# Kernel optimization log

Measured on AMD Instinct MI355X. Metric: run time of the kernel, lower is better.

## Reference

```python
import jax, jax.numpy as jnp
import numpy as np

ROPE_BASE = 10000.0
NUM_HEADS = 16
NUM_KV_HEADS = 4


def _rms_norm(x, eps):
    # F.rms_norm with no weight: x / sqrt(mean(x^2) + eps)
    return x * jax.lax.rsqrt(jnp.mean(x * x, axis=-1, keepdims=True) + eps)


def _apply_rope(x, cos, sin):
    h = x.shape[-1] // 2
    x1, x2 = x[..., :h], x[..., h:]
    return jnp.concatenate([x1 * cos + x2 * sin, -x1 * sin + x2 * cos], axis=-1)


def setup_inputs() -> dict:
    key = jax.random.key(0)
    ks = jax.random.split(key, 5)
    B, T, D = 2, 2048, 1024
    H, Hkv = NUM_HEADS, NUM_KV_HEADS
    hd = D // H
    kv_dim = Hkv * hd
    s_in = 1.0 / np.sqrt(D)
    return {
        "x": jax.random.normal(ks[0], (B, T, D), dtype=jnp.float32),
        "Wq": jax.random.normal(ks[1], (D, D), dtype=jnp.float32) * s_in,
        "Wk": jax.random.normal(ks[2], (kv_dim, D), dtype=jnp.float32) * s_in,
        "Wv": jax.random.normal(ks[3], (kv_dim, D), dtype=jnp.float32) * s_in,
        "Wproj": jax.random.normal(ks[4], (D, D), dtype=jnp.float32) * s_in,
        "q_gain": jnp.full((H,), 1.0, dtype=jnp.float32),
    }


def reference(x, Wq, Wk, Wv, Wproj, q_gain):
    B, T, D = x.shape
    H, Hkv = NUM_HEADS, NUM_KV_HEADS
    hd = D // H
    rep = H // Hkv
    eps = jnp.finfo(x.dtype).eps

    # QKV projections (F.linear: x @ W.T)
    q = jnp.einsum('btd,od->bto', x, Wq).reshape(B, T, H, hd).transpose(0, 2, 1, 3)
    k = jnp.einsum('btd,od->bto', x, Wk).reshape(B, T, Hkv, hd).transpose(0, 2, 1, 3)
    v = jnp.einsum('btd,od->bto', x, Wv).reshape(B, T, Hkv, hd).transpose(0, 2, 1, 3)

    q = _rms_norm(q, eps)
    k = _rms_norm(k, eps)

    # RoPE tables: [1, 1, T, hd/2]
    inv_freq = 1.0 / (ROPE_BASE ** (jnp.arange(0, hd, 2, dtype=jnp.float32) / hd))
    f = jnp.arange(T, dtype=jnp.float32)[:, None] * inv_freq[None, :]
    cos = jnp.cos(f)[None, None].astype(q.dtype)
    sin = jnp.sin(f)[None, None].astype(q.dtype)
    q = _apply_rope(q, cos, sin)
    k = _apply_rope(k, cos, sin)

    q = q * q_gain.astype(q.dtype)[None, :, None, None]

    # GQA without materializing repeated K/V: group q heads [Hkv, rep]
    qg = q.reshape(B, Hkv, rep, T, hd)
    scale = hd ** -0.5
    scores = jnp.einsum('bgrqd,bgkd->bgrqk', qg, k) * scale
    causal = jnp.tril(jnp.ones((T, T), dtype=bool))
    scores = jnp.where(causal, scores, -jnp.inf)
    att = jax.nn.softmax(scores.astype(jnp.float32), axis=-1).astype(q.dtype)
    y = jnp.einsum('bgrqk,bgkd->bgrqd', att, v)  # [B,Hkv,rep,T,hd]
    y = y.reshape(B, H, T, hd).transpose(0, 2, 1, 3).reshape(B, T, D)
    return jnp.einsum('btd,od->bto', y, Wproj)
```

## Files before the change

kernel.cpp:

```cpp
#include <hip/hip_runtime.h>
#include <cstdint>
#include <cstddef>

typedef __attribute__((ext_vector_type(8))) short short8;
typedef __attribute__((ext_vector_type(4))) float floatx4;
typedef __attribute__((ext_vector_type(4))) short short4v;
typedef unsigned short u16;
typedef unsigned int u32;

#define B_   2
#define T_   2048
#define D_   1024
#define H_   16
#define HKV_ 4
#define HD_  64
#define KV_  256
#define M_   4096
#define QS_  1536

#define NX   4194304
#define NWQ  1048576
#define NWK  262144
#define NWV  262144
#define NWP  1048576
#define NCAST (NX + NWQ + NWK + NWV + NWP)
#define CAST_BLOCKS (NCAST / 1024)
#define TAB_BLOCKS  256

__device__ __forceinline__ float b2f(u16 u) {
    union { u32 i; float f; } v; v.i = ((u32)u) << 16; return v.f;
}
__device__ __forceinline__ u16 f2b(float f) {
    union { float f; u32 i; } v; v.f = f;
    u32 r = v.i + 0x7FFF + ((v.i >> 16) & 1);
    return (u16)(r >> 16);
}
__device__ __forceinline__ u32 pack_hi(float a, float b) {
    union { float f; u32 u; } ua, ub; ua.f = a; ub.f = b;
    return (ua.u >> 16) | (ub.u & 0xFFFF0000u);
}

__device__ __forceinline__ void async16(const u16* g, u16* l) {
    __builtin_amdgcn_global_load_lds(
        (const __attribute__((address_space(1))) u32*)g,
        (__attribute__((address_space(3))) u32*)l, 16, 0, 0);
}

__global__ __launch_bounds__(256) void prep(const float* __restrict__ x,
                                            const float* __restrict__ wq,
                                            const float* __restrict__ wk,
                                            const float* __restrict__ wv,
                                            const float* __restrict__ wp,
                                            u16* __restrict__ dst,
                                            float2* __restrict__ tab) {
    int blk = blockIdx.x;
    if (blk < CAST_BLOCKS) {
        int i = blk * 1024 + threadIdx.x * 4;
        const float* src; int off;
        if      (i < NX)                  { src = x;  off = i; }
        else if (i < NX+NWQ)              { src = wq; off = i - NX; }
        else if (i < NX+NWQ+NWK)          { src = wk; off = i - (NX+NWQ); }
        else if (i < NX+NWQ+NWK+NWV)      { src = wv; off = i - (NX+NWQ+NWK); }
        else                              { src = wp; off = i - (NX+NWQ+NWK+NWV); }
        float4 v = *(const float4*)(src + off);
        short4v o;
        o.x = (short)f2b(v.x); o.y = (short)f2b(v.y);
        o.z = (short)f2b(v.z); o.w = (short)f2b(v.w);
        *(short4v*)(dst + i) = o;
    } else {
        int idx = (blk - CAST_BLOCKS) * 256 + threadIdx.x;
        int t = idx >> 5, i = idx & 31;
        float freq = exp2f(-(float)i * (13.287712379549449f / 32.0f));
        float ang = (float)t * freq;
        tab[idx] = make_float2(cosf(ang), sinf(ang));
    }
}

__global__ __launch_bounds__(256, 3) void gemm_qkv(const u16* __restrict__ A,
                                                   const u16* __restrict__ W,
                                                   u16* __restrict__ C,
                                                   u16* __restrict__ Vt,
                                                   const float* __restrict__ gain,
                                                   const float2* __restrict__ tab) {
    const int K = D_;
    __shared__ u16 As[2][2][128 * 32];
    __shared__ u16 Bs[2][2][64 * 32];
    const int t = threadIdx.x;
    const int wave = t >> 6, lane = t & 63;
    const int quad = lane >> 4, l16 = lane & 15;
    const int wm = wave * 32;
    const int m0 = blockIdx.y * 128, n0 = blockIdx.x * 64;

    floatx4 acc[2][4];
#pragma unroll
    for (int i = 0; i < 2; i++)
#pragma unroll
        for (int j = 0; j < 4; j++) acc[i][j] = (floatx4){0.f, 0.f, 0.f, 0.f};

    const int sr = t >> 2, sc = (t & 3) * 8;
    const u16* ga = A + (size_t)(m0 + sr) * K + sc;
    const u16* gb = W + (size_t)(n0 + sr) * K + sc;

    auto stage = [&](int buf, int half, int koff) {
        async16(ga + koff, As[buf][half] + t * 8);
        async16(ga + koff + (size_t)64 * K, As[buf][half] + t * 8 + 64 * 32);
        async16(gb + koff, Bs[buf][half] + t * 8);
    };

    stage(0, 0, 0);
    stage(0, 1, 32);

    int cur = 0;
    for (int kt = 0; kt < K; kt += 64) {
        __syncthreads();
        if (kt + 64 < K) {
            stage(cur ^ 1, 0, kt + 64);
            stage(cur ^ 1, 1, kt + 96);
        }
#pragma unroll
        for (int half = 0; half < 2; half++) {
            short8 af[2], bf[4];
#pragma unroll
            for (int mt = 0; mt < 2; mt++)
                af[mt] = *(const short8*)(As[cur][half] + (wm + mt * 16 + l16) * 32 + quad * 8);
#pragma unroll
            for (int nt = 0; nt < 4; nt++)
                bf[nt] = *(const short8*)(Bs[cur][half] + (nt * 16 + l16) * 32 + quad * 8);
#pragma unroll
            for (int mt = 0; mt < 2; mt++)
#pragma unroll
                for (int nt = 0; nt < 4; nt++)
                    acc[mt][nt] = __builtin_amdgcn_mfma_f32_16x16x32_bf16(
                        af[mt], bf[nt], acc[mt][nt], 0, 0, 0);
        }
        cur ^= 1;
    }

    const int col0 = n0;
    if (col0 < 1280) {
        float gs = (col0 < 1024)
                 ? gain[col0 >> 6] * (0.125f * 1.4426950408889634f)
                 : 1.0f;
#pragma unroll
        for (int mt = 0; mt < 2; mt++)
#pragma unroll
            for (int r = 0; r < 4; r++) {
                int row = m0 + wm + mt * 16 + quad * 4 + r;
                int tt = row & (T_ - 1);
                float v0 = acc[mt][0][r], v1 = acc[mt][1][r];
                float v2 = acc[mt][2][r], v3 = acc[mt][3][r];
                float ss = v0 * v0 + v1 * v1 + v2 * v2 + v3 * v3;
                ss += __shfl_xor(ss, 1); ss += __shfl_xor(ss, 2);
                ss += __shfl_xor(ss, 4); ss += __shfl_xor(ss, 8);
                float inv = rsqrtf(ss * (1.0f / 64.0f) + 1.1920929e-7f);
                v0 *= inv; v1 *= inv; v2 *= inv; v3 *= inv;
                float2 cs0 = tab[tt * 32 + l16];
                float2 cs1 = tab[tt * 32 + 16 + l16];
                float o0 = (v0 * cs0.x + v2 * cs0.y) * gs;
                float o1 = (v1 * cs1.x + v3 * cs1.y) * gs;
                float o2 = (v2 * cs0.x - v0 * cs0.y) * gs;
                float o3 = (v3 * cs1.x - v1 * cs1.y) * gs;
                u16* cp = C + (size_t)row * QS_ + col0 + l16;
                cp[0]  = f2b(o0);
                cp[16] = f2b(o1);
                cp[32] = f2b(o2);
                cp[48] = f2b(o3);
            }
    } else {
        const int g = (col0 - 1280) >> 6;
#pragma unroll
        for (int mt = 0; mt < 2; mt++)
#pragma unroll
            for (int r = 0; r < 4; r++) {
                int row = m0 + wm + mt * 16 + quad * 4 + r;
                int tt = row & (T_ - 1);
                int bb = row >> 11;
#pragma unroll
                for (int nt = 0; nt < 4; nt++)
                    Vt[(size_t)((bb * 4 + g) * 64 + nt * 16 + l16) * T_ + tt] =
                        f2b(acc[mt][nt][r]);
            }
    }
}

__global__ __launch_bounds__(256, 3) void gemm_proj(const u16* __restrict__ A,
                                                    const u16* __restrict__ W,
                                                    float* __restrict__ C) {
    const int K = D_;
    __shared__ u16 As[2][2][128 * 32];
    __shared__ u16 Bs[2][2][64 * 32];
    const int t = threadIdx.x;
    const int wave = t >> 6, lane = t & 63;
    const int quad = lane >> 4, l16 = lane & 15;
    const int wm = wave * 32;
    const int m0 = blockIdx.y * 128, n0 = blockIdx.x * 64;

    floatx4 acc[2][4];
#pragma unroll
    for (int i = 0; i < 2; i++)
#pragma unroll
        for (int j = 0; j < 4; j++) acc[i][j] = (floatx4){0.f, 0.f, 0.f, 0.f};

    const int sr = t >> 2, sc = (t & 3) * 8;
    const u16* ga = A + (size_t)(m0 + sr) * K + sc;
    const u16* gb = W + (size_t)(n0 + sr) * K + sc;

    auto stage = [&](int buf, int half, int koff) {
        async16(ga + koff, As[buf][half] + t * 8);
        async16(ga + koff + (size_t)64 * K, As[buf][half] + t * 8 + 64 * 32);
        async16(gb + koff, Bs[buf][half] + t * 8);
    };

    stage(0, 0, 0);
    stage(0, 1, 32);

    int cur = 0;
    for (int kt = 0; kt < K; kt += 64) {
        __syncthreads();
        if (kt + 64 < K) {
            stage(cur ^ 1, 0, kt + 64);
            stage(cur ^ 1, 1, kt + 96);
        }
#pragma unroll
        for (int half = 0; half < 2; half++) {
            short8 af[2], bf[4];
#pragma unroll
            for (int mt = 0; mt < 2; mt++)
                af[mt] = *(const short8*)(As[cur][half] + (wm + mt * 16 + l16) * 32 + quad * 8);
#pragma unroll
            for (int nt = 0; nt < 4; nt++)
                bf[nt] = *(const short8*)(Bs[cur][half] + (nt * 16 + l16) * 32 + quad * 8);
#pragma unroll
            for (int mt = 0; mt < 2; mt++)
#pragma unroll
                for (int nt = 0; nt < 4; nt++)
                    acc[mt][nt] = __builtin_amdgcn_mfma_f32_16x16x32_bf16(
                        af[mt], bf[nt], acc[mt][nt], 0, 0, 0);
        }
        cur ^= 1;
    }

#pragma unroll
    for (int mt = 0; mt < 2; mt++)
#pragma unroll
        for (int nt = 0; nt < 4; nt++)
#pragma unroll
            for (int r = 0; r < 4; r++) {
                int row = m0 + wm + mt * 16 + quad * 4 + r;
                int col = n0 + nt * 16 + l16;
                C[(size_t)row * D_ + col] = acc[mt][nt][r];
            }
}

__global__ __launch_bounds__(256, 4) void flash(const u16* __restrict__ QKV,
                                                const u16* __restrict__ Vtr,
                                                u16* __restrict__ Y,
                                                float* __restrict__ Opart,
                                                float* __restrict__ Lpart) {
    const int u  = blockIdx.x;
    const int h  = blockIdx.y;
    const int b  = blockIdx.z;
    const int g  = h >> 2;
    const int w    = threadIdx.x >> 6;
    const int lane = threadIdx.x & 63;
    const int quad = lane >> 4, l16 = lane & 15;

    __shared__ u16 Kt[64 * 64];
    __shared__ u16 Vs[64 * 64];
    __shared__ __align__(16) u16 P[4][16][72];

    const int xp = u & 15;
    const int nseg = (u < 16) ? 2 : 1;
    const int buf  = (u < 16) ? 0 : 1;
    int m0s[2], k0s[2], k1s[2];
    if (u < 16) {
        m0s[0] = xp * 64;        k0s[0] = 0;  k1s[0] = xp + 1;
        m0s[1] = (31 - xp) * 64; k0s[1] = 16; k1s[1] = 32 - xp;
    } else {
        m0s[0] = (31 - xp) * 64; k0s[0] = 0;  k1s[0] = 16;
        m0s[1] = 0; k0s[1] = 0; k1s[1] = 0;
    }

    const int srow = w * 16 + (lane >> 3);
    const int sseg = (lane & 7) ^ ((lane >> 3) & 7);
    const u16* kgb = QKV + (size_t)(b * T_ + srow) * QS_ + D_ + g * 64 + sseg * 8;
    const u16* vgb = Vtr + (size_t)((b * 4 + g) * 64 + srow) * T_ + sseg * 8;
    u16* klds = Kt + w * 1024 + lane * 8;
    u16* vlds = Vs + w * 1024 + lane * 8;
    const int sw0 = (quad ^ (l16 & 7)) * 8;
    const int sw1 = ((4 + quad) ^ (l16 & 7)) * 8;

    auto stage = [&](int tile) {
        const u16* kg = kgb + (size_t)tile * 64 * QS_;
        const u16* vg = vgb + (size_t)tile * 64;
        async16(kg, klds);
        async16(kg + (size_t)8 * QS_, klds + 512);
        async16(vg, vlds);
        async16(vg + (size_t)8 * T_, vlds + 512);
    };

    short8 ones;
#pragma unroll
    for (int i = 0; i < 8; i++) ones[i] = (short)0x3F80;

    stage(k0s[0]);

    for (int seg = 0; seg < nseg; ++seg) {
        const int mseg = m0s[seg], k0 = k0s[seg], k1 = k1s[seg];
        const int jt = mseg >> 6;
        const int m = mseg + w * 16;

        const u16* qp = QKV + (size_t)(b * T_ + m + l16) * QS_ + h * HD_ + quad * 8;
        short8 aq0 = *(const short8*)(qp);
        short8 aq1 = *(const short8*)(qp + 32);

        floatx4 acc[4];
#pragma unroll
        for (int i = 0; i < 4; i++) acc[i] = (floatx4){0.f, 0.f, 0.f, 0.f};
        floatx4 lAcc = (floatx4){0.f, 0.f, 0.f, 0.f};

        for (int tk = k0; tk < k1; ++tk) {
            __syncthreads();

            floatx4 S[4];
#pragma unroll
            for (int nt = 0; nt < 4; nt++) {
                const u16* kr = Kt + (nt * 16 + l16) * 64;
                short8 kf0 = *(const short8*)(kr + sw0);
                short8 kf1 = *(const short8*)(kr + sw1);
                S[nt] = (floatx4){0.f, 0.f, 0.f, 0.f};
                S[nt] = __builtin_amdgcn_mfma_f32_16x16x32_bf16(kf0, aq0, S[nt], 0, 0, 0);
                S[nt] = __builtin_amdgcn_mfma_f32_16x16x32_bf16(kf1, aq1, S[nt], 0, 0, 0);
            }
            short8 vf[4][2];
#pragma unroll
            for (int dd = 0; dd < 4; dd++) {
                const u16* vr = Vs + (dd * 16 + l16) * 64;
                vf[dd][0] = *(const short8*)(vr + sw0);
                vf[dd][1] = *(const short8*)(vr + sw1);
            }
            __syncthreads();

            int nxt = (tk + 1 < k1) ? tk + 1 : ((seg + 1 < nseg) ? k0s[seg + 1] : -1);
            if (nxt >= 0) stage(nxt);

            const bool msk = (tk == jt);
            const int qq = m + l16;
#pragma unroll
            for (int nt = 0; nt < 4; nt++) {
                float p[4];
#pragma unroll
                for (int r = 0; r < 4; r++) {
                    float e = __builtin_amdgcn_exp2f(S[nt][r]);
                    if (msk) {
                        int key = tk * 64 + nt * 16 + quad * 4 + r;
                        e = (key <= qq) ? e : 0.f;
                    }
                    p[r] = e;
                }
                uint2 pw; pw.x = pack_hi(p[0], p[1]); pw.y = pack_hi(p[2], p[3]);
                *(uint2*)&P[w][l16][nt * 16 + quad * 4] = pw;
            }
            short8 pf0 = *(const short8*)&P[w][l16][quad * 8];
            short8 pf1 = *(const short8*)&P[w][l16][quad * 8 + 32];
#pragma unroll
            for (int dd = 0; dd < 4; dd++) {
                acc[dd] = __builtin_amdgcn_mfma_f32_16x16x32_bf16(pf0, vf[dd][0], acc[dd], 0, 0, 0);
                acc[dd] = __builtin_amdgcn_mfma_f32_16x16x32_bf16(pf1, vf[dd][1], acc[dd], 0, 0, 0);
            }
            lAcc = __builtin_amdgcn_mfma_f32_16x16x32_bf16(pf0, ones, lAcc, 0, 0, 0);
            lAcc = __builtin_amdgcn_mfma_f32_16x16x32_bf16(pf1, ones, lAcc, 0, 0, 0);
        }

        if (u < 16 && seg == 0) {
#pragma unroll
            for (int r = 0; r < 4; r++) {
                float inv = 1.0f / lAcc[r];
                int row = m + quad * 4 + r;
                u16* yp = Y + (size_t)(b * T_ + row) * D_ + h * HD_ + l16;
#pragma unroll
                for (int dd = 0; dd < 4; dd++)
                    yp[dd * 16] = f2b(acc[dd][r] * inv);
            }
        } else {
#pragma unroll
            for (int r = 0; r < 4; r++) {
                int rp = m + quad * 4 + r - 1024;
                float* op = Opart + ((size_t)((buf * 2 + b) * 1024 + rp)) * 1024
                          + h * HD_ + l16;
#pragma unroll
                for (int dd = 0; dd < 4; dd++)
                    op[dd * 16] = acc[dd][r];
                if (l16 == 0)
                    Lpart[((buf * 2 + b) * 1024 + rp) * 16 + h] = lAcc[r];
            }
        }
    }
}

__global__ __launch_bounds__(256) void combine(const float* __restrict__ Opart,
                                               const float* __restrict__ Lpart,
                                               u16* __restrict__ Y) {
    int e = (blockIdx.x * 256 + threadIdx.x) * 4;
    int b = e >> 20;
    int rem = e & 1048575;
    int row = rem >> 10, col = rem & 1023;
    int li = (b * 1024 + row) * 16 + (col >> 6);
    float l0 = Lpart[li];
    float l1 = Lpart[li + 2 * 1024 * 16];
    float inv = 1.0f / (l0 + l1);
    size_t oi = ((size_t)(b * 1024 + row)) * 1024 + col;
    float4 o0 = *(const float4*)(Opart + oi);
    float4 o1 = *(const float4*)(Opart + oi + (size_t)2 * 1024 * 1024);
    short4v y;
    y.x = (short)f2b((o0.x + o1.x) * inv); y.y = (short)f2b((o0.y + o1.y) * inv);
    y.z = (short)f2b((o0.z + o1.z) * inv); y.w = (short)f2b((o0.w + o1.w) * inv);
    *(short4v*)(Y + (size_t)(b * T_ + 1024 + row) * D_ + col) = y;
}

extern "C" void kernel_launch(void* const* d_in, const int* in_sizes, int n_in,
                              void* d_out, int out_size, void* d_ws, size_t ws_size,
                              hipStream_t stream) {
    const float* x    = (const float*)d_in[0];
    const float* Wq   = (const float*)d_in[1];
    const float* Wk   = (const float*)d_in[2];
    const float* Wv   = (const float*)d_in[3];
    const float* Wp   = (const float*)d_in[4];
    const float* gain = (const float*)d_in[5];
    float* out = (float*)d_out;

    u16* xb   = (u16*)d_ws;
    u16* Wcat = xb + (size_t)NX;
    u16* Wpb  = Wcat + (size_t)(NWQ + NWK + NWV);
    u16* QKV  = Wpb + (size_t)NWP;
    u16* Vt   = QKV + (size_t)M_ * QS_;
    u16* Y    = Vt + (size_t)M_ * KV_;
    float2* tab = (float2*)(Y + (size_t)M_ * D_);
    float* Opart = (float*)(tab + 65536);
    float* Lpart = Opart + (size_t)4 * 1024 * 1024;

    prep<<<CAST_BLOCKS + TAB_BLOCKS, 256, 0, stream>>>(x, Wq, Wk, Wv, Wp, xb, tab);

    gemm_qkv<<<dim3(QS_ / 64, M_ / 128), 256, 0, stream>>>(xb, Wcat, QKV, Vt,
                                                           gain, tab);

    flash<<<dim3(32, H_, B_), 256, 0, stream>>>(QKV, Vt, Y, Opart, Lpart);

    combine<<<2048, 256, 0, stream>>>(Opart, Lpart, Y);

    gemm_proj<<<dim3(D_ / 64, M_ / 128), 256, 0, stream>>>(Y, Wpb, out);
}
```

Measured before the change: 158.9 us.

## Rework flash attention with 32x32 MFMA, 128-row blocks and triple-buffered K/V

The flash kernel now processes 128 query rows per block, each wave handling 32 rows with 32x32x16 bf16 MFMA. P is repacked in registers via cvt_pk and permlane32 swaps instead of going through LDS, and the row sum is accumulated in scalar adds rather than an extra MFMA. K/V tiles are triple-buffered with explicit vmcnt waits and MFMA regions are raised with setprio. Each block pairs a short and a long causal segment. Both segments are always written as partials through an LDS-transposed coalesced store, so combine now runs over all rows. This trades more partial-output traffic and lower occupancy (launch bounds 2) for fewer LDS round trips and larger MFMA tiles.

```diff
diff --git a/kernel.cpp b/kernel.cpp
--- a/kernel.cpp
+++ b/kernel.cpp
@@ -4,6 +4,7 @@
 
 typedef __attribute__((ext_vector_type(8))) short short8;
 typedef __attribute__((ext_vector_type(4))) float floatx4;
+typedef __attribute__((ext_vector_type(16))) float floatx16;
 typedef __attribute__((ext_vector_type(4))) short short4v;
 typedef unsigned short u16;
 typedef unsigned int u32;
@@ -44,6 +45,23 @@
     __builtin_amdgcn_global_load_lds(
         (const __attribute__((address_space(1))) u32*)g,
         (__attribute__((address_space(3))) u32*)l, 16, 0, 0);
+}
+
+__device__ __forceinline__ u32 cvtpk(float lo, float hi) {
+    u32 r;
+    asm("v_cvt_pk_bf16_f32 %0, %1, %2" : "=v"(r) : "v"(lo), "v"(hi));
+    return r;
+}
+__device__ __forceinline__ void swap32(u32& a, u32& b) {
+    asm volatile("v_permlane32_swap_b32 %0, %1" : "+v"(a), "+v"(b));
+}
+__device__ __forceinline__ void swap32f(float& a, float& b) {
+    asm volatile("v_permlane32_swap_b32 %0, %1" : "+v"(a), "+v"(b));
+}
+__device__ __forceinline__ short8 pkfrag(u32 w0, u32 w1, u32 w2, u32 w3) {
+    union { u32 w[4]; short8 s; } u;
+    u.w[0] = w0; u.w[1] = w1; u.w[2] = w2; u.w[3] = w3;
+    return u.s;
 }
 
 __global__ __launch_bounds__(256) void prep(const float* __restrict__ x,
@@ -252,9 +270,8 @@
             }
 }
 
-__global__ __launch_bounds__(256, 4) void flash(const u16* __restrict__ QKV,
+__global__ __launch_bounds__(256, 2) void flash(const u16* __restrict__ QKV,
                                                 const u16* __restrict__ Vtr,
-                                                u16* __restrict__ Y,
                                                 float* __restrict__ Opart,
                                                 float* __restrict__ Lpart) {
     const int u  = blockIdx.x;
@@ -263,138 +280,165 @@
     const int g  = h >> 2;
     const int w    = threadIdx.x >> 6;
     const int lane = threadIdx.x & 63;
-    const int quad = lane >> 4, l16 = lane & 15;
-
-    __shared__ u16 Kt[64 * 64];
-    __shared__ u16 Vs[64 * 64];
-    __shared__ __align__(16) u16 P[4][16][72];
-
-    const int xp = u & 15;
-    const int nseg = (u < 16) ? 2 : 1;
-    const int buf  = (u < 16) ? 0 : 1;
-    int m0s[2], k0s[2], k1s[2];
-    if (u < 16) {
-        m0s[0] = xp * 64;        k0s[0] = 0;  k1s[0] = xp + 1;
-        m0s[1] = (31 - xp) * 64; k0s[1] = 16; k1s[1] = 32 - xp;
-    } else {
-        m0s[0] = (31 - xp) * 64; k0s[0] = 0;  k1s[0] = 16;
-        m0s[1] = 0; k0s[1] = 0; k1s[1] = 0;
-    }
+    const int ln31 = lane & 31;
+    const int hi   = lane >> 5;
+    const int swz  = lane & 7;
+
+    __shared__ u16 Kb[3][4096];
+    __shared__ u16 Vb[3][4096];
+    __shared__ float Ot[4][2048];
 
     const int srow = w * 16 + (lane >> 3);
     const int sseg = (lane & 7) ^ ((lane >> 3) & 7);
     const u16* kgb = QKV + (size_t)(b * T_ + srow) * QS_ + D_ + g * 64 + sseg * 8;
     const u16* vgb = Vtr + (size_t)((b * 4 + g) * 64 + srow) * T_ + sseg * 8;
-    u16* klds = Kt + w * 1024 + lane * 8;
-    u16* vlds = Vs + w * 1024 + lane * 8;
-    const int sw0 = (quad ^ (l16 & 7)) * 8;
-    const int sw1 = ((4 + quad) ^ (l16 & 7)) * 8;
-
-    auto stage = [&](int tile) {
+
+    auto stage = [&](int tile, int bi) {
         const u16* kg = kgb + (size_t)tile * 64 * QS_;
         const u16* vg = vgb + (size_t)tile * 64;
-        async16(kg, klds);
-        async16(kg + (size_t)8 * QS_, klds + 512);
-        async16(vg, vlds);
-        async16(vg + (size_t)8 * T_, vlds + 512);
+        u16* kl = &Kb[bi][w * 1024 + lane * 8];
+        u16* vl = &Vb[bi][w * 1024 + lane * 8];
+        async16(kg, kl);
+        async16(kg + (size_t)8 * QS_, kl + 512);
+        async16(vg, vl);
+        async16(vg + (size_t)8 * T_, vl + 512);
     };
-
-    short8 ones;
-#pragma unroll
-    for (int i = 0; i < 8; i++) ones[i] = (short)0x3F80;
-
-    stage(k0s[0]);
-
-    for (int seg = 0; seg < nseg; ++seg) {
-        const int mseg = m0s[seg], k0 = k0s[seg], k1 = k1s[seg];
-        const int jt = mseg >> 6;
-        const int m = mseg + w * 16;
-
-        const u16* qp = QKV + (size_t)(b * T_ + m + l16) * QS_ + h * HD_ + quad * 8;
-        short8 aq0 = *(const short8*)(qp);
-        short8 aq1 = *(const short8*)(qp + 32);
-
-        floatx4 acc[4];
-#pragma unroll
-        for (int i = 0; i < 4; i++) acc[i] = (floatx4){0.f, 0.f, 0.f, 0.f};
-        floatx4 lAcc = (floatx4){0.f, 0.f, 0.f, 0.f};
-
-        for (int tk = k0; tk < k1; ++tk) {
-            __syncthreads();
-
-            floatx4 S[4];
-#pragma unroll
-            for (int nt = 0; nt < 4; nt++) {
-                const u16* kr = Kt + (nt * 16 + l16) * 64;
-                short8 kf0 = *(const short8*)(kr + sw0);
-                short8 kf1 = *(const short8*)(kr + sw1);
-                S[nt] = (floatx4){0.f, 0.f, 0.f, 0.f};
-                S[nt] = __builtin_amdgcn_mfma_f32_16x16x32_bf16(kf0, aq0, S[nt], 0, 0, 0);
-                S[nt] = __builtin_amdgcn_mfma_f32_16x16x32_bf16(kf1, aq1, S[nt], 0, 0, 0);
-            }
-            short8 vf[4][2];
-#pragma unroll
-            for (int dd = 0; dd < 4; dd++) {
-                const u16* vr = Vs + (dd * 16 + l16) * 64;
-                vf[dd][0] = *(const short8*)(vr + sw0);
-                vf[dd][1] = *(const short8*)(vr + sw1);
-            }
-            __syncthreads();
-
-            int nxt = (tk + 1 < k1) ? tk + 1 : ((seg + 1 < nseg) ? k0s[seg + 1] : -1);
-            if (nxt >= 0) stage(nxt);
-
-            const bool msk = (tk == jt);
-            const int qq = m + l16;
-#pragma unroll
-            for (int nt = 0; nt < 4; nt++) {
-                float p[4];
-#pragma unroll
-                for (int r = 0; r < 4; r++) {
-                    float e = __builtin_amdgcn_exp2f(S[nt][r]);
-                    if (msk) {
-                        int key = tk * 64 + nt * 16 + quad * 4 + r;
-                        e = (key <= qq) ? e : 0.f;
+    auto tileOf = [&](int gidx) { return (gidx <= u) ? gidx : gidx + 15 - 2 * u; };
+
+    stage(tileOf(0), 0);
+    stage(tileOf(1), 1);
+
+    int gi = 0;
+    for (int seg = 0; seg < 2; ++seg) {
+        const int jt   = seg ? 15 - u : u;
+        const int nIt  = seg ? 16 - u : u + 1;
+        const int qrow = jt * 128 + w * 32 + ln31;
+
+        const u16* qp = QKV + (size_t)(b * T_ + qrow) * QS_ + h * HD_;
+        short8 aq[4];
+#pragma unroll
+        for (int kc = 0; kc < 4; kc++)
+            aq[kc] = *(const short8*)(qp + kc * 16 + hi * 8);
+
+        floatx16 acc[2];
+#pragma unroll
+        for (int dh = 0; dh < 2; dh++)
+#pragma unroll
+            for (int i = 0; i < 16; i++) acc[dh][i] = 0.f;
+        float l = 0.f;
+
+        for (int itn = 0; itn < nIt; ++itn, ++gi) {
+            const int tk = tileOf(gi);
+            if (gi == 16) asm volatile("s_waitcnt vmcnt(0)" ::: "memory");
+            else          asm volatile("s_waitcnt vmcnt(4)" ::: "memory");
+            __builtin_amdgcn_s_barrier();
+            asm volatile("" ::: "memory");
+
+            const int bc = gi % 3;
+            if (gi + 2 <= 16) stage(tileOf(gi + 2), (gi + 2) % 3);
+
+            const u16* Kp = &Kb[bc][0];
+            const u16* Vp = &Vb[bc][0];
+            short8 kf[2][4], vfr[2][4];
+#pragma unroll
+            for (int kh = 0; kh < 2; kh++)
+#pragma unroll
+                for (int kc = 0; kc < 4; kc++)
+                    kf[kh][kc] = *(const short8*)(Kp + (kh * 32 + ln31) * 64 +
+                                                  (((kc * 2 + hi) ^ swz) << 3));
+#pragma unroll
+            for (int dh = 0; dh < 2; dh++)
+#pragma unroll
+                for (int kc = 0; kc < 4; kc++)
+                    vfr[dh][kc] = *(const short8*)(Vp + (dh * 32 + ln31) * 64 +
+                                                   (((kc * 2 + hi) ^ swz) << 3));
+
+            floatx16 s[2];
+#pragma unroll
+            for (int kh = 0; kh < 2; kh++)
+#pragma unroll
+                for (int i = 0; i < 16; i++) s[kh][i] = 0.f;
+
+            __builtin_amdgcn_s_setprio(1);
+#pragma unroll
+            for (int kc = 0; kc < 4; kc++) {
+                s[0] = __builtin_amdgcn_mfma_f32_32x32x16_bf16(kf[0][kc], aq[kc], s[0], 0, 0, 0);
+                s[1] = __builtin_amdgcn_mfma_f32_32x32x16_bf16(kf[1][kc], aq[kc], s[1], 0, 0, 0);
+            }
+            __builtin_amdgcn_s_setprio(0);
+
+            float p[2][16];
+            if (tk >= 2 * jt) {
+#pragma unroll
+                for (int kh = 0; kh < 2; kh++)
+#pragma unroll
+                    for (int r = 0; r < 16; r++) {
+                        int key = tk * 64 + kh * 32 + (r & 3) + ((r >> 2) << 3) + (hi << 2);
+                        float e = __builtin_amdgcn_exp2f(s[kh][r]);
+                        e = (key <= qrow) ? e : 0.f;
+                        l += e; p[kh][r] = e;
                     }
-                    p[r] = e;
-                }
-                uint2 pw; pw.x = pack_hi(p[0], p[1]); pw.y = pack_hi(p[2], p[3]);
-                *(uint2*)&P[w][l16][nt * 16 + quad * 4] = pw;
-            }
-            short8 pf0 = *(const short8*)&P[w][l16][quad * 8];
-            short8 pf1 = *(const short8*)&P[w][l16][quad * 8 + 32];
-#pragma unroll
-            for (int dd = 0; dd < 4; dd++) {
-                acc[dd] = __builtin_amdgcn_mfma_f32_16x16x32_bf16(pf0, vf[dd][0], acc[dd], 0, 0, 0);
-                acc[dd] = __builtin_amdgcn_mfma_f32_16x16x32_bf16(pf1, vf[dd][1], acc[dd], 0, 0, 0);
-            }
-            lAcc = __builtin_amdgcn_mfma_f32_16x16x32_bf16(pf0, ones, lAcc, 0, 0, 0);
-            lAcc = __builtin_amdgcn_mfma_f32_16x16x32_bf16(pf1, ones, lAcc, 0, 0, 0);
-        }
-
-        if (u < 16 && seg == 0) {
-#pragma unroll
-            for (int r = 0; r < 4; r++) {
-                float inv = 1.0f / lAcc[r];
-                int row = m + quad * 4 + r;
-                u16* yp = Y + (size_t)(b * T_ + row) * D_ + h * HD_ + l16;
-#pragma unroll
-                for (int dd = 0; dd < 4; dd++)
-                    yp[dd * 16] = f2b(acc[dd][r] * inv);
-            }
-        } else {
-#pragma unroll
-            for (int r = 0; r < 4; r++) {
-                int rp = m + quad * 4 + r - 1024;
-                float* op = Opart + ((size_t)((buf * 2 + b) * 1024 + rp)) * 1024
-                          + h * HD_ + l16;
-#pragma unroll
-                for (int dd = 0; dd < 4; dd++)
-                    op[dd * 16] = acc[dd][r];
-                if (l16 == 0)
-                    Lpart[((buf * 2 + b) * 1024 + rp) * 16 + h] = lAcc[r];
-            }
-        }
+            } else {
+#pragma unroll
+                for (int kh = 0; kh < 2; kh++)
+#pragma unroll
+                    for (int r = 0; r < 16; r++) {
+                        float e = __builtin_amdgcn_exp2f(s[kh][r]);
+                        l += e; p[kh][r] = e;
+                    }
+            }
+
+            short8 pb[4];
+#pragma unroll
+            for (int kh = 0; kh < 2; kh++) {
+                u32 a0 = cvtpk(p[kh][0], p[kh][1]),  b0 = cvtpk(p[kh][4], p[kh][5]);
+                u32 c0 = cvtpk(p[kh][2], p[kh][3]),  d0 = cvtpk(p[kh][6], p[kh][7]);
+                swap32(a0, b0); swap32(c0, d0);
+                pb[kh * 2] = pkfrag(a0, c0, b0, d0);
+                u32 a1 = cvtpk(p[kh][8],  p[kh][9]),  b1 = cvtpk(p[kh][12], p[kh][13]);
+                u32 c1 = cvtpk(p[kh][10], p[kh][11]), d1 = cvtpk(p[kh][14], p[kh][15]);
+                swap32(a1, b1); swap32(c1, d1);
+                pb[kh * 2 + 1] = pkfrag(a1, c1, b1, d1);
+            }
+
+            __builtin_amdgcn_s_setprio(1);
+#pragma unroll
+            for (int kc = 0; kc < 4; kc++) {
+                acc[0] = __builtin_amdgcn_mfma_f32_32x32x16_bf16(vfr[0][kc], pb[kc], acc[0], 0, 0, 0);
+                acc[1] = __builtin_amdgcn_mfma_f32_32x32x16_bf16(vfr[1][kc], pb[kc], acc[1], 0, 0, 0);
+            }
+            __builtin_amdgcn_s_setprio(0);
+        }
+
+        float la = l, lb = l;
+        swap32f(la, lb);
+        float lt = la + lb;
+
+        float* ot = &Ot[w][0];
+#pragma unroll
+        for (int dh = 0; dh < 2; dh++)
+#pragma unroll
+            for (int g4 = 0; g4 < 4; g4++) {
+                int ss = (dh * 8 + g4 * 2 + hi) ^ (ln31 & 7);
+                float4 v = make_float4(acc[dh][g4 * 4 + 0], acc[dh][g4 * 4 + 1],
+                                       acc[dh][g4 * 4 + 2], acc[dh][g4 * 4 + 3]);
+                *(float4*)(ot + ln31 * 64 + ss * 4) = v;
+            }
+        asm volatile("s_waitcnt lgkmcnt(0)" ::: "memory");
+
+        const int hq = lane >> 4;
+        const int s4 = lane & 15;
+        float* obase = Opart + (size_t)seg * 4194304 +
+                       ((size_t)(b * 2048 + jt * 128 + w * 32)) * 1024 + h * HD_;
+#pragma unroll
+        for (int it = 0; it < 8; it++) {
+            int q2 = it * 4 + hq;
+            int ss = s4 ^ (q2 & 7);
+            float4 v = *(const float4*)(ot + q2 * 64 + ss * 4);
+            *(float4*)(obase + (size_t)q2 * 1024 + s4 * 4) = v;
+        }
+        if (lane < 32)
+            Lpart[((size_t)seg * 4096 + b * 2048 + jt * 128 + w * 32 + lane) * 16 + h] = lt;
     }
 }
 
@@ -402,20 +446,18 @@
                                                const float* __restrict__ Lpart,
                                                u16* __restrict__ Y) {
     int e = (blockIdx.x * 256 + threadIdx.x) * 4;
-    int b = e >> 20;
-    int rem = e & 1048575;
-    int row = rem >> 10, col = rem & 1023;
-    int li = (b * 1024 + row) * 16 + (col >> 6);
+    int row = e >> 10, col = e & 1023;
+    int li = row * 16 + (col >> 6);
     float l0 = Lpart[li];
-    float l1 = Lpart[li + 2 * 1024 * 16];
+    float l1 = Lpart[li + 4096 * 16];
     float inv = 1.0f / (l0 + l1);
-    size_t oi = ((size_t)(b * 1024 + row)) * 1024 + col;
+    size_t oi = (size_t)row * 1024 + col;
     float4 o0 = *(const float4*)(Opart + oi);
-    float4 o1 = *(const float4*)(Opart + oi + (size_t)2 * 1024 * 1024);
+    float4 o1 = *(const float4*)(Opart + oi + (size_t)4194304);
     short4v y;
     y.x = (short)f2b((o0.x + o1.x) * inv); y.y = (short)f2b((o0.y + o1.y) * inv);
     y.z = (short)f2b((o0.z + o1.z) * inv); y.w = (short)f2b((o0.w + o1.w) * inv);
-    *(short4v*)(Y + (size_t)(b * T_ + 1024 + row) * D_ + col) = y;
+    *(short4v*)(Y + (size_t)row * D_ + col) = y;
 }
 
 extern "C" void kernel_launch(void* const* d_in, const int* in_sizes, int n_in,
@@ -437,16 +479,16 @@
     u16* Y    = Vt + (size_t)M_ * KV_;
     float2* tab = (float2*)(Y + (size_t)M_ * D_);
     float* Opart = (float*)(tab + 65536);
-    float* Lpart = Opart + (size_t)4 * 1024 * 1024;
+    float* Lpart = Opart + (size_t)8 * 1024 * 1024;
 
     prep<<<CAST_BLOCKS + TAB_BLOCKS, 256, 0, stream>>>(x, Wq, Wk, Wv, Wp, xb, tab);
 
     gemm_qkv<<<dim3(QS_ / 64, M_ / 128), 256, 0, stream>>>(xb, Wcat, QKV, Vt,
                                                            gain, tab);
 
-    flash<<<dim3(32, H_, B_), 256, 0, stream>>>(QKV, Vt, Y, Opart, Lpart);
-
-    combine<<<2048, 256, 0, stream>>>(Opart, Lpart, Y);
+    flash<<<dim3(16, H_, B_), 256, 0, stream>>>(QKV, Vt, Opart, Lpart);
+
+    combine<<<4096, 256, 0, stream>>>(Opart, Lpart, Y);
 
     gemm_proj<<<dim3(D_ / 64, M_ / 128), 256, 0, stream>>>(Y, Wpb, out);
 }
```

Result: slower. 164.5 us (+3.5%).

## Enlarge GEMM tiles to 128x128 with 2x2 wave layout and swizzled LDS

Applied to the files above, without the earlier changes.

Both the QKV and output-projection GEMMs now use 128x128 block tiles instead of 128x64. Each wave computes a 64x64 sub-tile with 4x4 MFMA accumulators. LDS loads and reads use an XOR swizzle on the k-chunk index to reduce bank conflicts. The goal is more operand reuse per LDS byte and fewer global loads, at the cost of higher register use (occupancy bound lowered to 2) and half as many blocks in the grid.

```diff
diff --git a/kernel.cpp b/kernel.cpp
--- a/kernel.cpp
+++ b/kernel.cpp
@@ -76,7 +76,7 @@
     }
 }
 
-__global__ __launch_bounds__(256, 3) void gemm_qkv(const u16* __restrict__ A,
+__global__ __launch_bounds__(256, 2) void gemm_qkv(const u16* __restrict__ A,
                                                    const u16* __restrict__ W,
                                                    u16* __restrict__ C,
                                                    u16* __restrict__ Vt,
@@ -84,27 +84,29 @@
                                                    const float2* __restrict__ tab) {
     const int K = D_;
     __shared__ u16 As[2][2][128 * 32];
-    __shared__ u16 Bs[2][2][64 * 32];
+    __shared__ u16 Bs[2][2][128 * 32];
     const int t = threadIdx.x;
     const int wave = t >> 6, lane = t & 63;
     const int quad = lane >> 4, l16 = lane & 15;
-    const int wm = wave * 32;
-    const int m0 = blockIdx.y * 128, n0 = blockIdx.x * 64;
-
-    floatx4 acc[2][4];
-#pragma unroll
-    for (int i = 0; i < 2; i++)
+    const int wr = (wave >> 1) * 64, wc = (wave & 1) * 64;
+    const int m0 = blockIdx.y * 128, n0 = blockIdx.x * 128;
+
+    floatx4 acc[4][4];
+#pragma unroll
+    for (int i = 0; i < 4; i++)
 #pragma unroll
         for (int j = 0; j < 4; j++) acc[i][j] = (floatx4){0.f, 0.f, 0.f, 0.f};
 
-    const int sr = t >> 2, sc = (t & 3) * 8;
+    const int sr = t >> 2;
+    const int sc = (((t & 3) ^ ((t >> 3) & 3)) * 8);
     const u16* ga = A + (size_t)(m0 + sr) * K + sc;
     const u16* gb = W + (size_t)(n0 + sr) * K + sc;
 
     auto stage = [&](int buf, int half, int koff) {
         async16(ga + koff, As[buf][half] + t * 8);
-        async16(ga + koff + (size_t)64 * K, As[buf][half] + t * 8 + 64 * 32);
+        async16(ga + koff + (size_t)64 * K, As[buf][half] + t * 8 + 2048);
         async16(gb + koff, Bs[buf][half] + t * 8);
+        async16(gb + koff + (size_t)64 * K, Bs[buf][half] + t * 8 + 2048);
     };
 
     stage(0, 0, 0);
@@ -119,15 +121,21 @@
         }
 #pragma unroll
         for (int half = 0; half < 2; half++) {
-            short8 af[2], bf[4];
-#pragma unroll
-            for (int mt = 0; mt < 2; mt++)
-                af[mt] = *(const short8*)(As[cur][half] + (wm + mt * 16 + l16) * 32 + quad * 8);
-#pragma unroll
-            for (int nt = 0; nt < 4; nt++)
-                bf[nt] = *(const short8*)(Bs[cur][half] + (nt * 16 + l16) * 32 + quad * 8);
-#pragma unroll
-            for (int mt = 0; mt < 2; mt++)
+            short8 af[4], bf[4];
+#pragma unroll
+            for (int mt = 0; mt < 4; mt++) {
+                int row = wr + mt * 16 + l16;
+                af[mt] = *(const short8*)(As[cur][half] + row * 32 +
+                                          ((quad ^ ((row >> 1) & 3)) << 3));
+            }
+#pragma unroll
+            for (int nt = 0; nt < 4; nt++) {
+                int row = wc + nt * 16 + l16;
+                bf[nt] = *(const short8*)(Bs[cur][half] + row * 32 +
+                                          ((quad ^ ((row >> 1) & 3)) << 3));
+            }
+#pragma unroll
+            for (int mt = 0; mt < 4; mt++)
 #pragma unroll
                 for (int nt = 0; nt < 4; nt++)
                     acc[mt][nt] = __builtin_amdgcn_mfma_f32_16x16x32_bf16(
@@ -136,16 +144,16 @@
         cur ^= 1;
     }
 
-    const int col0 = n0;
+    const int col0 = n0 + wc;
     if (col0 < 1280) {
         float gs = (col0 < 1024)
                  ? gain[col0 >> 6] * (0.125f * 1.4426950408889634f)
                  : 1.0f;
 #pragma unroll
-        for (int mt = 0; mt < 2; mt++)
+        for (int mt = 0; mt < 4; mt++)
 #pragma unroll
             for (int r = 0; r < 4; r++) {
-                int row = m0 + wm + mt * 16 + quad * 4 + r;
+                int row = m0 + wr + mt * 16 + quad * 4 + r;
                 int tt = row & (T_ - 1);
                 float v0 = acc[mt][0][r], v1 = acc[mt][1][r];
                 float v2 = acc[mt][2][r], v3 = acc[mt][3][r];
@@ -169,10 +177,10 @@
     } else {
         const int g = (col0 - 1280) >> 6;
 #pragma unroll
-        for (int mt = 0; mt < 2; mt++)
+        for (int mt = 0; mt < 4; mt++)
 #pragma unroll
             for (int r = 0; r < 4; r++) {
-                int row = m0 + wm + mt * 16 + quad * 4 + r;
+                int row = m0 + wr + mt * 16 + quad * 4 + r;
                 int tt = row & (T_ - 1);
                 int bb = row >> 11;
 #pragma unroll
@@ -183,32 +191,34 @@
     }
 }
 
-__global__ __launch_bounds__(256, 3) void gemm_proj(const u16* __restrict__ A,
+__global__ __launch_bounds__(256, 2) void gemm_proj(const u16* __restrict__ A,
                                                     const u16* __restrict__ W,
                                                     float* __restrict__ C) {
     const int K = D_;
     __shared__ u16 As[2][2][128 * 32];
-    __shared__ u16 Bs[2][2][64 * 32];
+    __shared__ u16 Bs[2][2][128 * 32];
     const int t = threadIdx.x;
     const int wave = t >> 6, lane = t & 63;
     const int quad = lane >> 4, l16 = lane & 15;
-    const int wm = wave * 32;
-    const int m0 = blockIdx.y * 128, n0 = blockIdx.x * 64;
-
-    floatx4 acc[2][4];
-#pragma unroll
-    for (int i = 0; i < 2; i++)
+    const int wr = (wave >> 1) * 64, wc = (wave & 1) * 64;
+    const int m0 = blockIdx.y * 128, n0 = blockIdx.x * 128;
+
+    floatx4 acc[4][4];
+#pragma unroll
+    for (int i = 0; i < 4; i++)
 #pragma unroll
         for (int j = 0; j < 4; j++) acc[i][j] = (floatx4){0.f, 0.f, 0.f, 0.f};
 
-    const int sr = t >> 2, sc = (t & 3) * 8;
+    const int sr = t >> 2;
+    const int sc = (((t & 3) ^ ((t >> 3) & 3)) * 8);
     const u16* ga = A + (size_t)(m0 + sr) * K + sc;
     const u16* gb = W + (size_t)(n0 + sr) * K + sc;
 
     auto stage = [&](int buf, int half, int koff) {
         async16(ga + koff, As[buf][half] + t * 8);
-        async16(ga + koff + (size_t)64 * K, As[buf][half] + t * 8 + 64 * 32);
+        async16(ga + koff + (size_t)64 * K, As[buf][half] + t * 8 + 2048);
         async16(gb + koff, Bs[buf][half] + t * 8);
+        async16(gb + koff + (size_t)64 * K, Bs[buf][half] + t * 8 + 2048);
     };
 
     stage(0, 0, 0);
@@ -223,15 +233,21 @@
         }
 #pragma unroll
         for (int half = 0; half < 2; half++) {
-            short8 af[2], bf[4];
-#pragma unroll
-            for (int mt = 0; mt < 2; mt++)
-                af[mt] = *(const short8*)(As[cur][half] + (wm + mt * 16 + l16) * 32 + quad * 8);
-#pragma unroll
-            for (int nt = 0; nt < 4; nt++)
-                bf[nt] = *(const short8*)(Bs[cur][half] + (nt * 16 + l16) * 32 + quad * 8);
-#pragma unroll
-            for (int mt = 0; mt < 2; mt++)
+            short8 af[4], bf[4];
+#pragma unroll
+            for (int mt = 0; mt < 4; mt++) {
+                int row = wr + mt * 16 + l16;
+                af[mt] = *(const short8*)(As[cur][half] + row * 32 +
+                                          ((quad ^ ((row >> 1) & 3)) << 3));
+            }
+#pragma unroll
+            for (int nt = 0; nt < 4; nt++) {
+                int row = wc + nt * 16 + l16;
+                bf[nt] = *(const short8*)(Bs[cur][half] + row * 32 +
+                                          ((quad ^ ((row >> 1) & 3)) << 3));
+            }
+#pragma unroll
+            for (int mt = 0; mt < 4; mt++)
 #pragma unroll
                 for (int nt = 0; nt < 4; nt++)
                     acc[mt][nt] = __builtin_amdgcn_mfma_f32_16x16x32_bf16(
@@ -241,13 +257,13 @@
     }
 
 #pragma unroll
-    for (int mt = 0; mt < 2; mt++)
+    for (int mt = 0; mt < 4; mt++)
 #pragma unroll
         for (int nt = 0; nt < 4; nt++)
 #pragma unroll
             for (int r = 0; r < 4; r++) {
-                int row = m0 + wm + mt * 16 + quad * 4 + r;
-                int col = n0 + nt * 16 + l16;
+                int row = m0 + wr + mt * 16 + quad * 4 + r;
+                int col = n0 + wc + nt * 16 + l16;
                 C[(size_t)row * D_ + col] = acc[mt][nt][r];
             }
 }
@@ -441,12 +457,12 @@
 
     prep<<<CAST_BLOCKS + TAB_BLOCKS, 256, 0, stream>>>(x, Wq, Wk, Wv, Wp, xb, tab);
 
-    gemm_qkv<<<dim3(QS_ / 64, M_ / 128), 256, 0, stream>>>(xb, Wcat, QKV, Vt,
-                                                           gain, tab);
+    gemm_qkv<<<dim3(QS_ / 128, M_ / 128), 256, 0, stream>>>(xb, Wcat, QKV, Vt,
+                                                            gain, tab);
 
     flash<<<dim3(32, H_, B_), 256, 0, stream>>>(QKV, Vt, Y, Opart, Lpart);
 
     combine<<<2048, 256, 0, stream>>>(Opart, Lpart, Y);
 
-    gemm_proj<<<dim3(D_ / 64, M_ / 128), 256, 0, stream>>>(Y, Wpb, out);
-}
+    gemm_proj<<<dim3(D_ / 128, M_ / 128), 256, 0, stream>>>(Y, Wpb, out);
+}
```

Result: no change. 159.9 us (+0.7%).
